# Performance work log

Measured on AMD Instinct MI355X. Metric: run time of the kernel, lower is better.

Reference implementation:

```python
import jax, jax.numpy as jnp
import numpy as np

H = 512          # hidden_size
E = 2 * H        # bidirectional embed dim
NH = 8           # attention heads
HD = E // NH     # head dim = 128
SEQ = 10         # hard-coded seq_len in forward
IN = 512         # input_size
OUT = 256        # output_size


def _gru_dir(gi, Whh, bhh, reverse):
    # gi: [B,S,3H] precomputed input-side gate pre-activations
    if reverse:
        gi = gi[:, ::-1]
    B = gi.shape[0]
    h0 = jnp.zeros((B, H), gi.dtype)

    def step(h, gi_t):
        gh = h @ Whh.T + bhh                      # [B,3H]
        ir, iz, inn = jnp.split(gi_t, 3, axis=-1)
        hr, hz, hn = jnp.split(gh, 3, axis=-1)
        r = jax.nn.sigmoid(ir + hr)
        z = jax.nn.sigmoid(iz + hz)
        n = jnp.tanh(inn + r * hn)
        h_new = (1.0 - z) * n + z * h
        return h_new, h_new

    _, hs = jax.lax.scan(step, h0, jnp.swapaxes(gi, 0, 1))
    hs = jnp.swapaxes(hs, 0, 1)                   # [B,S,H]
    if reverse:
        hs = hs[:, ::-1]
    return hs


def _bi_gru_layer(x_seq, Wih, Whh, bih, bhh):
    # Wih: [2, 3H, in]; dir 0 = forward, dir 1 = backward
    outs = []
    for d, rev in ((0, False), (1, True)):
        gi = jnp.einsum('bsi,gi->bsg', x_seq, Wih[d]) + bih[d]
        outs.append(_gru_dir(gi, Whh[d], bhh[d], rev))
    return jnp.concatenate(outs, axis=-1)         # [B,S,2H]


def _attention(x, in_proj_w, in_proj_b, out_proj_w, out_proj_b):
    B, S, _ = x.shape
    qkv = x @ in_proj_w.T + in_proj_b             # [B,S,3E]
    q, k, v = jnp.split(qkv, 3, axis=-1)
    q = q.reshape(B, S, NH, HD)
    k = k.reshape(B, S, NH, HD)
    v = v.reshape(B, S, NH, HD)
    scores = jnp.einsum('bqhd,bkhd->bhqk', q, k) / jnp.sqrt(jnp.asarray(HD, x.dtype))
    attn = jax.nn.softmax(scores, axis=-1)
    o = jnp.einsum('bhqk,bkhd->bqhd', attn, v).reshape(B, S, E)
    return o @ out_proj_w.T + out_proj_b


def _forward(x, Wp, bp, Wih0, Whh0, bih0, bhh0, Wih1, Whh1, bih1, bhh1,
             in_proj_w, in_proj_b, out_proj_w, out_proj_b, W1, b1, W2, b2):
    x_proj = x @ Wp.T + bp                        # [B,H]
    phases = 2.0 * np.pi * np.arange(SEQ) / SEQ
    cos = jnp.asarray(np.cos(phases), x.dtype)    # [S]
    sin = jnp.asarray(np.sin(phases), x.dtype)
    rolled = jnp.roll(x_proj, shift=1, axis=-1)
    x_seq = (x_proj[:, None, :] * (1.0 + 0.1 * cos[None, :, None])
             + 0.05 * sin[None, :, None] * rolled[:, None, :])  # [B,S,H]
    h1 = _bi_gru_layer(x_seq, Wih0, Whh0, bih0, bhh0)           # [B,S,2H]
    gru_out = _bi_gru_layer(h1, Wih1, Whh1, bih1, bhh1)         # [B,S,2H]
    attn_out = _attention(gru_out, in_proj_w, in_proj_b, out_proj_w, out_proj_b)
    aggregated = jnp.mean(gru_out + attn_out, axis=1)           # [B,2H]
    hid = jnp.tanh(aggregated @ W1.T + b1)                      # [B,128]
    return hid @ W2.T + b2                                      # [B,OUT]


def setup_inputs() -> dict:
    key = jax.random.key(0)
    ks = jax.random.split(key, 24)
    s = 1.0 / np.sqrt(H)
    u = lambda k, shape: jax.random.uniform(k, shape, jnp.float32, -s, s)
    return {
        'x': jax.random.normal(ks[0], (4096, IN), jnp.float32),
        'Wp': u(ks[1], (H, IN)), 'bp': u(ks[2], (H,)),
        'Wih0': u(ks[3], (2, 3 * H, H)), 'Whh0': u(ks[4], (2, 3 * H, H)),
        'bih0': u(ks[5], (2, 3 * H)), 'bhh0': u(ks[6], (2, 3 * H)),
        'Wih1': u(ks[7], (2, 3 * H, 2 * H)), 'Whh1': u(ks[8], (2, 3 * H, H)),
        'bih1': u(ks[9], (2, 3 * H)), 'bhh1': u(ks[10], (2, 3 * H)),
        'in_proj_w': u(ks[11], (3 * E, E)), 'in_proj_b': u(ks[12], (3 * E,)),
        'out_proj_w': u(ks[13], (E, E)), 'out_proj_b': u(ks[14], (E,)),
        'W1': u(ks[15], (128, E)), 'b1': u(ks[16], (128,)),
        'W2': u(ks[17], (OUT, 128)), 'b2': u(ks[18], (OUT,)),
    }


def reference(x, Wp, bp, Wih0, Whh0, bih0, bhh0, Wih1, Whh1, bih1, bhh1,
              in_proj_w, in_proj_b, out_proj_w, out_proj_b, W1, b1, W2, b2):
    return _forward(x, Wp, bp, Wih0, Whh0, bih0, bhh0, Wih1, Whh1, bih1, bhh1,
                    in_proj_w, in_proj_b, out_proj_w, out_proj_b, W1, b1, W2, b2)
```

## Files before the change

kernel.cpp:

```cpp
#include <hip/hip_runtime.h>
#include <math.h>


#define SEQ 10

typedef unsigned short bf16u;
typedef __attribute__((ext_vector_type(8))) short short8v;
typedef __attribute__((ext_vector_type(4))) float f32x4;

#define AS1 __attribute__((address_space(1)))
#define AS3 __attribute__((address_space(3)))

__device__ __forceinline__ float b2f(bf16u u) {
    union { unsigned int i; float f; } v; v.i = ((unsigned int)u) << 16; return v.f;
}
__device__ __forceinline__ bf16u f2b(float f) {
    union { float f; unsigned int i; } v; v.f = f;
    unsigned int r = (v.i + 0x7FFFu + ((v.i >> 16) & 1u)) >> 16;
    return (bf16u)r;
}
__device__ __forceinline__ float fast_sigm(float x) { return 1.0f / (1.0f + __expf(-x)); }
__device__ __forceinline__ float fast_tanh(float x) {
    float e = __expf(-2.0f * x);
    return 2.0f / (1.0f + e) - 1.0f;
}

__global__ void cvt_f2b(const float* __restrict__ src, bf16u* __restrict__ dst, int n4)
{
    int i = blockIdx.x * 256 + threadIdx.x;
    if (i < n4) {
        float4 v = ((const float4*)src)[i];
        ushort4 u; u.x = f2b(v.x); u.y = f2b(v.y); u.z = f2b(v.z); u.w = f2b(v.w);
        ((ushort4*)dst)[i] = u;
    }
}

template <typename TC>
__global__ __launch_bounds__(512) void gemm_mfma256(
    const bf16u* __restrict__ A, long long sAz, int lda,
    const bf16u* __restrict__ W, long long sWz,
    const float* __restrict__ bias, long long sBz,
    TC* __restrict__ C, long long sCz, int ldc,
    int K, int act)
{
    __shared__ bf16u As[2][256 * 64];
    __shared__ bf16u Ws[2][256 * 64];

    const int z = blockIdx.z;
    A += (long long)z * sAz;
    W += (long long)z * sWz;
    C += (long long)z * sCz;
    const float* bz = bias ? (bias + (long long)z * sBz) : nullptr;

    const int gx = gridDim.x;
    const int nwg = gx * gridDim.y;
    const int orig = blockIdx.y * gx + blockIdx.x;
    const int q = nwg >> 3, rres = nwg & 7;
    const int xcd = orig & 7, loc = orig >> 3;
    const int wgid = (xcd < rres ? xcd * (q + 1) : rres * (q + 1) + (xcd - rres) * q) + loc;
    const int bm = (wgid / gx) * 256;
    const int bn = (wgid % gx) * 256;

    const int tid = threadIdx.x;
    const int lane = tid & 63;
    const int w = tid >> 6;
    const int wm = w >> 2;
    const int wn = w & 3;
    const int l15 = lane & 15;
    const int lk8 = (lane >> 4) * 8;
    const int swz = (l15 & 7) << 3;

    f32x4 acc[8][4];
#pragma unroll
    for (int i = 0; i < 8; ++i)
#pragma unroll
        for (int j = 0; j < 4; ++j)
#pragma unroll
            for (int r = 0; r < 4; ++r) acc[i][j][r] = 0.0f;

    const int srow = lane >> 3;
    const int scol = ((lane & 7) ^ srow) * 8;
    const bf16u* Ag[4];
    const bf16u* Wg[4];
    int loff[4];
#pragma unroll
    for (int p = 0; p < 4; ++p) {
        const int r = p * 64 + w * 8 + srow;
        Ag[p] = A + (long long)(bm + r) * lda + scol;
        Wg[p] = W + (long long)(bn + r) * K + scol;
        loff[p] = (p * 8 + w) * 512;
    }

    auto stage = [&](int kt, int b) {
        const long long k1 = (long long)kt << 6;
#pragma unroll
        for (int p = 0; p < 4; ++p) {
            __builtin_amdgcn_global_load_lds((const AS1 void*)(Ag[p] + k1),
                (AS3 void*)(&As[b][loff[p]]), 16, 0, 0);
            __builtin_amdgcn_global_load_lds((const AS1 void*)(Wg[p] + k1),
                (AS3 void*)(&Ws[b][loff[p]]), 16, 0, 0);
        }
    };
    auto compute = [&](int b) {
#pragma unroll
        for (int ks = 0; ks < 2; ++ks) {
            const int ko = (ks * 32 + lk8) ^ swz;
            short8v af[8], bfr[4];
#pragma unroll
            for (int i = 0; i < 8; ++i)
                af[i] = *(const short8v*)(&As[b][(wm * 128 + i * 16 + l15) * 64 + ko]);
#pragma unroll
            for (int i = 0; i < 4; ++i)
                bfr[i] = *(const short8v*)(&Ws[b][(wn * 64 + i * 16 + l15) * 64 + ko]);
#pragma unroll
            for (int mi = 0; mi < 8; ++mi)
#pragma unroll
                for (int ni = 0; ni < 4; ++ni)
                    acc[mi][ni] = __builtin_amdgcn_mfma_f32_16x16x32_bf16(
                        af[mi], bfr[ni], acc[mi][ni], 0, 0, 0);
        }
    };

    const int nt = K >> 6;

    stage(0, 0);
    stage(1, 1);

    for (int t = 0; t < nt - 1; ++t) {
        asm volatile("s_waitcnt vmcnt(8)" ::: "memory");
        __builtin_amdgcn_s_barrier();
        asm volatile("" ::: "memory");
        compute(t & 1);
        asm volatile("" ::: "memory");
        __builtin_amdgcn_s_barrier();
        if (t + 2 < nt) stage(t + 2, t & 1);
    }
    asm volatile("s_waitcnt vmcnt(0)" ::: "memory");
    __builtin_amdgcn_s_barrier();
    compute((nt - 1) & 1);

    const int r0 = (lane >> 4) * 4;
#pragma unroll
    for (int mi = 0; mi < 8; ++mi) {
#pragma unroll
        for (int ni = 0; ni < 4; ++ni) {
            const int col = bn + wn * 64 + ni * 16 + l15;
            float badd = bz ? bz[col] : 0.0f;
#pragma unroll
            for (int r = 0; r < 4; ++r) {
                const long long row = bm + wm * 128 + mi * 16 + r0 + r;
                float v = acc[mi][ni][r] + badd;
                if (act) v = tanhf(v);
                if constexpr (sizeof(TC) == 4) ((float*)C)[row * ldc + col] = v;
                else                           ((bf16u*)C)[row * ldc + col] = f2b(v);
            }
        }
    }
}

template <typename TC>
__global__ __launch_bounds__(256) void gemm_mfma128p(
    const bf16u* __restrict__ A, long long sAz, int lda,
    const bf16u* __restrict__ W, long long sWz,
    const float* __restrict__ bias, long long sBz,
    TC* __restrict__ C, long long sCz, int ldc,
    int K, int act)
{
    __shared__ bf16u As[2][128 * 64];
    __shared__ bf16u Ws[2][128 * 64];

    const int z = blockIdx.z;
    A += (long long)z * sAz;
    W += (long long)z * sWz;
    C += (long long)z * sCz;
    const float* bz = bias ? (bias + (long long)z * sBz) : nullptr;

    const int gx = gridDim.x;
    const int nwg = gx * gridDim.y;
    const int orig = blockIdx.y * gx + blockIdx.x;
    const int q = nwg >> 3, rres = nwg & 7;
    const int xcd = orig & 7, loc = orig >> 3;
    const int wgid = (xcd < rres ? xcd * (q + 1) : rres * (q + 1) + (xcd - rres) * q) + loc;
    const int bm = (wgid / gx) * 128;
    const int bn = (wgid % gx) * 128;

    const int tid = threadIdx.x;
    const int lane = tid & 63;
    const int w = tid >> 6;
    const int wm = w >> 1;
    const int wn = w & 1;
    const int l15 = lane & 15;
    const int lk8 = (lane >> 4) * 8;
    const int swz = (l15 & 7) << 3;

    f32x4 acc[4][4];
#pragma unroll
    for (int i = 0; i < 4; ++i)
#pragma unroll
        for (int j = 0; j < 4; ++j)
#pragma unroll
            for (int r = 0; r < 4; ++r) acc[i][j][r] = 0.0f;

    const int srow = lane >> 3;
    const int scol = ((lane & 7) ^ srow) * 8;
    const bf16u* Ag[4];
    const bf16u* Wg[4];
    int loff[4];
#pragma unroll
    for (int p = 0; p < 4; ++p) {
        const int r = p * 32 + w * 8 + srow;
        Ag[p] = A + (long long)(bm + r) * lda + scol;
        Wg[p] = W + (long long)(bn + r) * K + scol;
        loff[p] = (p * 32 + w * 8) * 64;
    }

    auto stage = [&](int kt, int b) {
        const long long k1 = (long long)kt << 6;
#pragma unroll
        for (int p = 0; p < 4; ++p) {
            __builtin_amdgcn_global_load_lds((const AS1 void*)(Ag[p] + k1),
                (AS3 void*)(&As[b][loff[p]]), 16, 0, 0);
            __builtin_amdgcn_global_load_lds((const AS1 void*)(Wg[p] + k1),
                (AS3 void*)(&Ws[b][loff[p]]), 16, 0, 0);
        }
    };
    auto compute = [&](int b) {
#pragma unroll
        for (int ks = 0; ks < 2; ++ks) {
            const int ko = (ks * 32 + lk8) ^ swz;
            short8v af[4], bfr[4];
#pragma unroll
            for (int i = 0; i < 4; ++i)
                af[i] = *(const short8v*)(&As[b][(wm * 64 + i * 16 + l15) * 64 + ko]);
#pragma unroll
            for (int i = 0; i < 4; ++i)
                bfr[i] = *(const short8v*)(&Ws[b][(wn * 64 + i * 16 + l15) * 64 + ko]);
            __builtin_amdgcn_s_setprio(1);
#pragma unroll
            for (int mi = 0; mi < 4; ++mi)
#pragma unroll
                for (int ni = 0; ni < 4; ++ni)
                    acc[mi][ni] = __builtin_amdgcn_mfma_f32_16x16x32_bf16(
                        af[mi], bfr[ni], acc[mi][ni], 0, 0, 0);
            __builtin_amdgcn_s_setprio(0);
        }
    };

    const int nt = K >> 6;

    stage(0, 0);
    stage(1, 1);

    for (int t = 0; t < nt - 1; ++t) {
        asm volatile("s_waitcnt vmcnt(8)" ::: "memory");
        __builtin_amdgcn_s_barrier();
        asm volatile("" ::: "memory");
        compute(t & 1);
        asm volatile("" ::: "memory");
        __builtin_amdgcn_s_barrier();
        if (t + 2 < nt) stage(t + 2, t & 1);
    }
    asm volatile("s_waitcnt vmcnt(0)" ::: "memory");
    __builtin_amdgcn_s_barrier();
    compute((nt - 1) & 1);

    const int r0 = (lane >> 4) * 4;
#pragma unroll
    for (int mi = 0; mi < 4; ++mi) {
#pragma unroll
        for (int ni = 0; ni < 4; ++ni) {
            const int col = bn + wn * 64 + ni * 16 + l15;
            float badd = bz ? bz[col] : 0.0f;
#pragma unroll
            for (int r = 0; r < 4; ++r) {
                const long long row = bm + wm * 64 + mi * 16 + r0 + r;
                float v = acc[mi][ni][r] + badd;
                if (act) v = tanhf(v);
                if constexpr (sizeof(TC) == 4) ((float*)C)[row * ldc + col] = v;
                else                           ((bf16u*)C)[row * ldc + col] = f2b(v);
            }
        }
    }
}

template <typename TC>
__global__ __launch_bounds__(256) void gemm_mfma(
    const bf16u* __restrict__ A, long long sAz, int lda,
    const bf16u* __restrict__ W, long long sWz,
    const float* __restrict__ bias, long long sBz,
    TC* __restrict__ C, long long sCz, int ldc,
    int K, int act)
{
    __shared__ bf16u As[128 * 64];
    __shared__ bf16u Ws[128 * 64];

    const int z = blockIdx.z;
    A += (long long)z * sAz;
    W += (long long)z * sWz;
    C += (long long)z * sCz;
    const float* bz = bias ? (bias + (long long)z * sBz) : nullptr;

    const int gx = gridDim.x;
    const int nwg = gx * gridDim.y;
    const int orig = blockIdx.y * gx + blockIdx.x;
    const int q = nwg >> 3, rres = nwg & 7;
    const int xcd = orig & 7, loc = orig >> 3;
    const int wgid = (xcd < rres ? xcd * (q + 1) : rres * (q + 1) + (xcd - rres) * q) + loc;
    const int bm = (wgid / gx) * 128;
    const int bn = (wgid % gx) * 128;

    const int tid = threadIdx.x;
    const int lane = tid & 63;
    const int wave = tid >> 6;
    const int wr = (wave >> 1) * 64;
    const int wc = (wave & 1) * 64;
    const int l15 = lane & 15;
    const int lk8 = (lane >> 4) * 8;

    f32x4 acc[4][4];
#pragma unroll
    for (int i = 0; i < 4; ++i)
#pragma unroll
        for (int j = 0; j < 4; ++j)
#pragma unroll
            for (int r = 0; r < 4; ++r) acc[i][j][r] = 0.0f;

    const int sr = wave * 32 + (lane >> 3);
    const int sc = (lane & 7) * 8;
    const bf16u* Ag = A + (long long)(bm + sr) * lda + sc;
    const bf16u* Wg = W + (long long)(bn + sr) * K + sc;
    bf16u* Al = As + wave * 32 * 64;
    bf16u* Wl = Ws + wave * 32 * 64;

    for (int k0 = 0; k0 < K; k0 += 64) {
#pragma unroll
        for (int p = 0; p < 4; ++p) {
            __builtin_amdgcn_global_load_lds(
                (const AS1 void*)(Ag + k0 + (long long)(8 * p) * lda),
                (AS3 void*)(Al + 8 * p * 64), 16, 0, 0);
            __builtin_amdgcn_global_load_lds(
                (const AS1 void*)(Wg + k0 + (long long)(8 * p) * K),
                (AS3 void*)(Wl + 8 * p * 64), 16, 0, 0);
        }
        __syncthreads();
#pragma unroll
        for (int ks = 0; ks < 2; ++ks) {
            short8v af[4], bfr[4];
#pragma unroll
            for (int i = 0; i < 4; ++i)
                af[i] = *(const short8v*)(As + (wr + i * 16 + l15) * 64 + ks * 32 + lk8);
#pragma unroll
            for (int i = 0; i < 4; ++i)
                bfr[i] = *(const short8v*)(Ws + (wc + i * 16 + l15) * 64 + ks * 32 + lk8);
#pragma unroll
            for (int mi = 0; mi < 4; ++mi)
#pragma unroll
                for (int ni = 0; ni < 4; ++ni)
                    acc[mi][ni] = __builtin_amdgcn_mfma_f32_16x16x32_bf16(
                        af[mi], bfr[ni], acc[mi][ni], 0, 0, 0);
        }
        __syncthreads();
    }

    const int r0 = (lane >> 4) * 4;
#pragma unroll
    for (int mi = 0; mi < 4; ++mi) {
#pragma unroll
        for (int ni = 0; ni < 4; ++ni) {
            const int col = bn + wc + ni * 16 + l15;
            float badd = bz ? bz[col] : 0.0f;
#pragma unroll
            for (int r = 0; r < 4; ++r) {
                const long long row = bm + wr + mi * 16 + r0 + r;
                float v = acc[mi][ni][r] + badd;
                if (act) v = tanhf(v);
                if constexpr (sizeof(TC) == 4) ((float*)C)[row * ldc + col] = v;
                else                           ((bf16u*)C)[row * ldc + col] = f2b(v);
            }
        }
    }
}

template <int LAYER, bool FIRST>
__global__ __launch_bounds__(256) void gru_step(
    const bf16u* __restrict__ Hb,
    const bf16u* __restrict__ Whh,
    const float* __restrict__ bhh,
    const bf16u* __restrict__ P0,
    const bf16u* __restrict__ P1,
    const float* __restrict__ bih,
    const bf16u* __restrict__ GIT,
    const float* __restrict__ hprev,
    float* __restrict__ hnext,
    bf16u* __restrict__ hnextb,
    bf16u* __restrict__ hout,
    int t, int CB)
{
    __shared__ bf16u As[2][64 * 64];
    __shared__ bf16u Ws[2][96 * 64];

    const int z = blockIdx.z;
    const int bn = blockIdx.x * 32;
    const int bm = blockIdx.y * 64;
    const int tid = threadIdx.x;
    const int lane = tid & 63;
    const int wave = tid >> 6;
    const int wm = wave >> 1;
    const int wn = wave & 1;
    const int l15 = lane & 15;
    const int lk8 = (lane >> 4) * 8;
    const int swz = (l15 & 7) << 3;

    f32x4 acc[3][2];
#pragma unroll
    for (int g = 0; g < 3; ++g)
#pragma unroll
        for (int i = 0; i < 2; ++i)
#pragma unroll
            for (int r = 0; r < 4; ++r) acc[g][i][r] = 0.0f;

    if constexpr (!FIRST) {
        const bf16u* hsrc = Hb + (long long)z * CB * 512;
        const bf16u* wsrc = Whh + (long long)z * 1536 * 512;

        const int srow = lane >> 3;
        const int sc = ((lane & 7) ^ srow) * 8;
        const bf16u* Ag = hsrc + (long long)(bm + 16 * wave + srow) * 512 + sc;
        const bf16u* Wg[3];
#pragma unroll
        for (int p = 0; p < 3; ++p) {
            const int lr = 24 * wave + 8 * p + srow;
            const int g = lr >> 5, c = lr & 31;
            Wg[p] = wsrc + (long long)(g * 512 + bn + c) * 512 + sc;
        }

        auto stage = [&](int kt, int b) {
            const long long k0 = (long long)kt << 6;
#pragma unroll
            for (int p = 0; p < 2; ++p)
                __builtin_amdgcn_global_load_lds(
                    (const AS1 void*)(Ag + k0 + (long long)(8 * p) * 512),
                    (AS3 void*)(&As[b][(16 * wave + 8 * p) * 64]), 16, 0, 0);
#pragma unroll
            for (int p = 0; p < 3; ++p)
                __builtin_amdgcn_global_load_lds(
                    (const AS1 void*)(Wg[p] + k0),
                    (AS3 void*)(&Ws[b][(24 * wave + 8 * p) * 64]), 16, 0, 0);
        };
        auto compute = [&](int b) {
#pragma unroll
            for (int ks = 0; ks < 2; ++ks) {
                const int ko = (ks * 32 + lk8) ^ swz;
                short8v af[2], bf[3];
#pragma unroll
                for (int mi = 0; mi < 2; ++mi)
                    af[mi] = *(const short8v*)(&As[b][(wm * 32 + mi * 16 + l15) * 64 + ko]);
#pragma unroll
                for (int g = 0; g < 3; ++g)
                    bf[g] = *(const short8v*)(&Ws[b][(g * 32 + wn * 16 + l15) * 64 + ko]);
                __builtin_amdgcn_s_setprio(1);
#pragma unroll
                for (int g = 0; g < 3; ++g)
#pragma unroll
                    for (int mi = 0; mi < 2; ++mi)
                        acc[g][mi] = __builtin_amdgcn_mfma_f32_16x16x32_bf16(
                            af[mi], bf[g], acc[g][mi], 0, 0, 0);
                __builtin_amdgcn_s_setprio(0);
            }
        };

        stage(0, 0);
        stage(1, 1);
        for (int kt = 0; kt < 7; ++kt) {
            asm volatile("s_waitcnt vmcnt(5)" ::: "memory");
            __builtin_amdgcn_s_barrier();
            asm volatile("" ::: "memory");
            compute(kt & 1);
            asm volatile("" ::: "memory");
            __builtin_amdgcn_s_barrier();
            if (kt + 2 < 8) stage(kt + 2, kt & 1);
        }
        asm volatile("s_waitcnt vmcnt(0)" ::: "memory");
        __builtin_amdgcn_s_barrier();
        compute(1);
    }

    const int r0 = (lane >> 4) * 4;
    const int s = z ? (SEQ - 1 - t) : t;
    float c0 = 0.0f, c1 = 0.0f;
    if (LAYER == 0) {
        float ph = 0.6283185307179586f * (float)s;
        c0 = 1.0f + 0.1f * cosf(ph);
        c1 = 0.05f * sinf(ph);
    }

    const int j = bn + wn * 16 + l15;
    const float bh0 = bhh[z * 1536 + j];
    const float bh1 = bhh[z * 1536 + 512 + j];
    const float bh2 = bhh[z * 1536 + 1024 + j];
    float bi0 = 0, bi1 = 0, bi2 = 0;
    if (LAYER == 0) {
        bi0 = bih[z * 1536 + j];
        bi1 = bih[z * 1536 + 512 + j];
        bi2 = bih[z * 1536 + 1024 + j];
    }

#pragma unroll
    for (int mi = 0; mi < 2; ++mi) {
#pragma unroll
        for (int rr = 0; rr < 4; ++rr) {
            const int m = bm + wm * 32 + mi * 16 + r0 + rr;
            float gr = acc[0][mi][rr] + bh0;
            float gz = acc[1][mi][rr] + bh1;
            float gn = acc[2][mi][rr] + bh2;
            float ir, iz, inn;
            if (LAYER == 0) {
                const bf16u* p0 = P0 + (long long)m * 3072 + z * 1536 + j;
                const bf16u* p1 = P1 + (long long)m * 3072 + z * 1536 + j;
                ir  = c0 * b2f(p0[0])    + c1 * b2f(p1[0])    + bi0;
                iz  = c0 * b2f(p0[512])  + c1 * b2f(p1[512])  + bi1;
                inn = c0 * b2f(p0[1024]) + c1 * b2f(p1[1024]) + bi2;
            } else {
                const bf16u* gi = GIT + (((long long)z * CB + m) * SEQ + s) * 1536 + j;
                ir = b2f(gi[0]); iz = b2f(gi[512]); inn = b2f(gi[1024]);
            }
            const long long ho = ((long long)z * CB + m) * 512 + j;
            float r  = fast_sigm(ir + gr);
            float zz = fast_sigm(iz + gz);
            float n  = fast_tanh(inn + r * gn);
            float hnew;
            if constexpr (FIRST) hnew = (1.0f - zz) * n;
            else                 hnew = (1.0f - zz) * n + zz * hprev[ho];
            hnext[ho]  = hnew;
            hnextb[ho] = f2b(hnew);
            hout[((long long)m * SEQ + s) * 1024 + z * 512 + j] = f2b(hnew);
        }
    }
}

__global__ void roll_b(const bf16u* __restrict__ xp, bf16u* __restrict__ rl)
{
    int idx = blockIdx.x * 256 + threadIdx.x;
    int i = idx & 511;
    int b = idx >> 9;
    rl[(size_t)b * 512 + i] = xp[(size_t)b * 512 + ((i + 511) & 511)];
}

__global__ __launch_bounds__(128) void attn_kernel(const bf16u* __restrict__ qkv,
                                                   bf16u* __restrict__ o)
{
    const int bh = blockIdx.x;
    const int h = bh & 7;
    const int bl = bh >> 3;
    const int tid = threadIdx.x;

    __shared__ float Q[SEQ][128], Kx[SEQ][128], V[SEQ][128], Amat[SEQ][SEQ];

    const bf16u* base = qkv + (size_t)bl * SEQ * 3072 + h * 128;
#pragma unroll
    for (int s = 0; s < SEQ; ++s) {
        Q[s][tid]  = b2f(base[s * 3072 + tid]);
        Kx[s][tid] = b2f(base[s * 3072 + 1024 + tid]);
        V[s][tid]  = b2f(base[s * 3072 + 2048 + tid]);
    }
    __syncthreads();

    if (tid < SEQ * SEQ) {
        int q = tid / SEQ, k = tid % SEQ;
        float acc = 0.0f;
#pragma unroll 8
        for (int d0 = 0; d0 < 128; ++d0) acc += Q[q][d0] * Kx[k][d0];
        Amat[q][k] = acc * 0.08838834764831845f;
    }
    __syncthreads();

    if (tid < SEQ) {
        float m = -1e30f;
#pragma unroll
        for (int k = 0; k < SEQ; ++k) m = fmaxf(m, Amat[tid][k]);
        float e[SEQ], ssum = 0.0f;
#pragma unroll
        for (int k = 0; k < SEQ; ++k) { e[k] = expf(Amat[tid][k] - m); ssum += e[k]; }
        float inv = 1.0f / ssum;
#pragma unroll
        for (int k = 0; k < SEQ; ++k) Amat[tid][k] = e[k] * inv;
    }
    __syncthreads();

    bf16u* ob = o + (size_t)bl * SEQ * 1024 + h * 128;
#pragma unroll
    for (int q = 0; q < SEQ; ++q) {
        float acc = 0.0f;
#pragma unroll
        for (int k = 0; k < SEQ; ++k) acc += Amat[q][k] * V[k][tid];
        ob[q * 1024 + tid] = f2b(acc);
    }
}

__global__ void mean_kernel(const bf16u* __restrict__ go, const bf16u* __restrict__ ao,
                            bf16u* __restrict__ agg)
{
    int idx = blockIdx.x * 256 + threadIdx.x;
    int j4 = (idx & 255) * 4;
    int bl = idx >> 8;
    const bf16u* g = go + (size_t)bl * (SEQ * 1024) + j4;
    const bf16u* a = ao + (size_t)bl * (SEQ * 1024) + j4;
    float s0 = 0, s1 = 0, s2 = 0, s3 = 0;
#pragma unroll
    for (int t = 0; t < SEQ; ++t) {
        ushort4 gv = *(const ushort4*)(g + t * 1024);
        ushort4 av = *(const ushort4*)(a + t * 1024);
        s0 += b2f(gv.x) + b2f(av.x);
        s1 += b2f(gv.y) + b2f(av.y);
        s2 += b2f(gv.z) + b2f(av.z);
        s3 += b2f(gv.w) + b2f(av.w);
    }
    ushort4 u; u.x = f2b(0.1f * s0); u.y = f2b(0.1f * s1); u.z = f2b(0.1f * s2); u.w = f2b(0.1f * s3);
    *(ushort4*)(agg + (size_t)bl * 1024 + j4) = u;
}

extern "C" void kernel_launch(void* const* d_in, const int* in_sizes, int n_in,
                              void* d_out, int out_size, void* d_ws, size_t ws_size,
                              hipStream_t stream)
{
    const float* x    = (const float*)d_in[0];
    const float* Wp   = (const float*)d_in[1];
    const float* bp   = (const float*)d_in[2];
    const float* Wih0 = (const float*)d_in[3];
    const float* Whh0 = (const float*)d_in[4];
    const float* bih0 = (const float*)d_in[5];
    const float* bhh0 = (const float*)d_in[6];
    const float* Wih1 = (const float*)d_in[7];
    const float* Whh1 = (const float*)d_in[8];
    const float* bih1 = (const float*)d_in[9];
    const float* bhh1 = (const float*)d_in[10];
    const float* ipw  = (const float*)d_in[11];
    const float* ipb  = (const float*)d_in[12];
    const float* opw  = (const float*)d_in[13];
    const float* opb  = (const float*)d_in[14];
    const float* W1   = (const float*)d_in[15];
    const float* b1   = (const float*)d_in[16];
    const float* W2   = (const float*)d_in[17];
    const float* b2   = (const float*)d_in[18];
    float* out = (float*)d_out;

    const long long WOVER = 9437184LL;
    const long long WALL  = 24969216LL;
    int CB = 0;
    for (int c = 4096; c >= 128; c >>= 1)
        if (WOVER + (long long)c * 114688 <= (long long)ws_size) { CB = c; break; }
    if (CB == 0) return;
    const bool resident = (WALL + (long long)CB * 114688 <= (long long)ws_size);
    const long long WB = resident ? WALL : WOVER;
    const int CBA = CB / 2;

    bf16u* wreg = (bf16u*)d_ws;
    bf16u *Wpb, *Wih0b, *Whh0b, *Wih1b, *Whh1b, *ipwb, *opwb, *W1b, *W2b;
    if (resident) {
        Wpb   = wreg;
        Wih0b = wreg + 262144;
        Whh0b = wreg + 1835008;
        Wih1b = wreg + 3407872;
        Whh1b = wreg + 6553600;
        ipwb  = wreg + 8126464;
        opwb  = wreg + 11272192;
        W1b   = wreg + 12320768;
        W2b   = wreg + 12451840;
    } else {
        Wpb   = wreg;
        Wih0b = wreg + 262144;
        Whh0b = wreg + 1835008;
        Wih1b = wreg;
        Whh1b = wreg + 3145728;
        ipwb  = wreg;
        opwb  = wreg + 3145728;
        W1b   = wreg + 4194304;
        W2b   = wreg + 4325376;
    }

    char* A0 = (char*)d_ws + WB;
    bf16u* H1c = (bf16u*)A0;
    bf16u* GOc = (bf16u*)(A0 + 20480LL * CB);
    char*  U   = A0 + 40960LL * CB;
    bf16u* P0    = (bf16u*)U;
    bf16u* P1    = (bf16u*)(U + 6144LL * CB);
    bf16u* XB    = (bf16u*)(U + 12288LL * CB);
    bf16u* XPb   = (bf16u*)(U + 13312LL * CB);
    bf16u* RLb   = (bf16u*)(U + 14336LL * CB);
    bf16u* GIT   = (bf16u*)U;
    char*  HC    = U + 61440LL * CB;
    bf16u* QKV   = (bf16u*)U;
    bf16u* OC    = (bf16u*)(U + 61440LL * CB);
    bf16u* AOC   = (bf16u*)A0;
    bf16u* AGGb  = (bf16u*)(A0 + 10240LL * CB);
    bf16u* HIDb  = (bf16u*)(A0 + 12288LL * CB);

    const dim3 blk(256);
    const int MB = CB / 128;

    auto cvt = [&](const float* s, bf16u* d, long long nfloats) {
        int n4 = (int)(nfloats / 4);
        cvt_f2b<<<(n4 + 255) / 256, blk, 0, stream>>>(s, d, n4);
    };

    if (resident) {
        cvt(Wp,   Wpb,   512LL * 512);
        cvt(Wih0, Wih0b, 2LL * 1536 * 512);
        cvt(Whh0, Whh0b, 2LL * 1536 * 512);
        cvt(Wih1, Wih1b, 2LL * 1536 * 1024);
        cvt(Whh1, Whh1b, 2LL * 1536 * 512);
        cvt(ipw,  ipwb,  3072LL * 1024);
        cvt(opw,  opwb,  1024LL * 1024);
        cvt(W1,   W1b,   128LL * 1024);
        cvt(W2,   W2b,   256LL * 128);
    }

    for (int c0 = 0; c0 < 4096; c0 += CB) {
        cvt(x + (long long)c0 * 512, XB, (long long)CB * 512);
        if (!resident) {
            cvt(Wp,   Wpb,   512LL * 512);
            cvt(Wih0, Wih0b, 2LL * 1536 * 512);
            cvt(Whh0, Whh0b, 2LL * 1536 * 512);
        }

        gemm_mfma<bf16u><<<dim3(4, MB, 1), blk, 0, stream>>>(
            XB, 0, 512, Wpb, 0, bp, 0, XPb, 0, 512, 512, 0);
        roll_b<<<CB * 2, blk, 0, stream>>>(XPb, RLb);
        gemm_mfma128p<bf16u><<<dim3(24, MB, 2), blk, 0, stream>>>(
            XPb, (long long)CB * 512, 512, Wih0b, 0, nullptr, 0,
            P0, (long long)CB * 3072, 3072, 512, 0);

        for (int t = 0; t < SEQ; ++t) {
            const int rb = t & 1;
            float* hprev  = (float*)(HC + (long long)rb * 6144 * CB);
            bf16u* Hbr    = (bf16u*)(HC + (long long)rb * 6144 * CB + 4096LL * CB);
            float* hnext  = (float*)(HC + (long long)(1 - rb) * 6144 * CB);
            bf16u* hnextb = (bf16u*)(HC + (long long)(1 - rb) * 6144 * CB + 4096LL * CB);
            if (t == 0)
                gru_step<0, true><<<dim3(16, CB / 64, 2), blk, 0, stream>>>(
                    Hbr, Whh0b, bhh0, P0, P1, bih0, nullptr,
                    hprev, hnext, hnextb, H1c, t, CB);
            else
                gru_step<0, false><<<dim3(16, CB / 64, 2), blk, 0, stream>>>(
                    Hbr, Whh0b, bhh0, P0, P1, bih0, nullptr,
                    hprev, hnext, hnextb, H1c, t, CB);
        }

        if (!resident) {
            cvt(Wih1, Wih1b, 2LL * 1536 * 1024);
            cvt(Whh1, Whh1b, 2LL * 1536 * 512);
        }
        gemm_mfma256<bf16u><<<dim3(6, CB * 10 / 256, 2), dim3(512), 0, stream>>>(
            H1c, 0, 1024, Wih1b, 1536LL * 1024, bih1, 1536,
            GIT, (long long)CB * SEQ * 1536, 1536, 1024, 0);

        for (int t = 0; t < SEQ; ++t) {
            const int rb = t & 1;
            float* hprev  = (float*)(HC + (long long)rb * 6144 * CB);
            bf16u* Hbr    = (bf16u*)(HC + (long long)rb * 6144 * CB + 4096LL * CB);
            float* hnext  = (float*)(HC + (long long)(1 - rb) * 6144 * CB);
            bf16u* hnextb = (bf16u*)(HC + (long long)(1 - rb) * 6144 * CB + 4096LL * CB);
            if (t == 0)
                gru_step<1, true><<<dim3(16, CB / 64, 2), blk, 0, stream>>>(
                    Hbr, Whh1b, bhh1, nullptr, nullptr, nullptr, GIT,
                    hprev, hnext, hnextb, GOc, t, CB);
            else
                gru_step<1, false><<<dim3(16, CB / 64, 2), blk, 0, stream>>>(
                    Hbr, Whh1b, bhh1, nullptr, nullptr, nullptr, GIT,
                    hprev, hnext, hnextb, GOc, t, CB);
        }

        if (!resident) {
            cvt(ipw, ipwb, 3072LL * 1024);
            cvt(opw, opwb, 1024LL * 1024);
            cvt(W1,  W1b,  128LL * 1024);
            cvt(W2,  W2b,  256LL * 128);
        }
        gemm_mfma256<bf16u><<<dim3(12, CB * 10 / 256, 1), dim3(512), 0, stream>>>(
            GOc, 0, 1024, ipwb, 0, ipb, 0, QKV, 0, 3072, 1024, 0);
        for (int a0 = 0; a0 < CB; a0 += CBA) {
            attn_kernel<<<CBA * 8, dim3(128), 0, stream>>>(
                QKV + (long long)a0 * 30720, OC);
            gemm_mfma128p<bf16u><<<dim3(8, CBA * 10 / 128, 1), blk, 0, stream>>>(
                OC, 0, 1024, opwb, 0, opb, 0, AOC, 0, 1024, 1024, 0);
            mean_kernel<<<CBA, blk, 0, stream>>>(
                GOc + (long long)a0 * 10240, AOC, AGGb + (long long)a0 * 1024);
        }
        gemm_mfma<bf16u><<<dim3(1, MB, 1), blk, 0, stream>>>(
            AGGb, 0, 1024, W1b, 0, b1, 0, HIDb, 0, 128, 1024, 1);
        gemm_mfma<float><<<dim3(2, MB, 1), blk, 0, stream>>>(
            HIDb, 0, 128, W2b, 0, b2, 0, out + (long long)c0 * 256, 0, 256, 128, 0);
    }
}
```

Measured before the change: 2.123 ms.

## Average attention output over sequence before out-projection to shrink GEMM

Because the output projection is linear, the mean over the sequence is taken inside the attention kernel, and the out-projection GEMM then runs on one row per batch element instead of ten. The attention output buffer, the chunked attention loop and the per-token AO reads in the mean kernel go away, and the projected result is written in fp32 and added to the GRU-output mean. This cuts the out-projection FLOPs and memory traffic by about the sequence length. It relies on gemm_mfma128p being instantiated with a float output and on the fp32 ATT buffer fitting within the reused region.

```diff
diff --git a/kernel.cpp b/kernel.cpp
--- a/kernel.cpp
+++ b/kernel.cpp
@@ -547,7 +547,7 @@
 }
 
 __global__ __launch_bounds__(128) void attn_kernel(const bf16u* __restrict__ qkv,
-                                                   bf16u* __restrict__ o)
+                                                   bf16u* __restrict__ osum)
 {
     const int bh = blockIdx.x;
     const int h = bh & 7;
@@ -587,35 +587,34 @@
     }
     __syncthreads();
 
-    bf16u* ob = o + (size_t)bl * SEQ * 1024 + h * 128;
+    float os = 0.0f;
 #pragma unroll
     for (int q = 0; q < SEQ; ++q) {
         float acc = 0.0f;
 #pragma unroll
         for (int k = 0; k < SEQ; ++k) acc += Amat[q][k] * V[k][tid];
-        ob[q * 1024 + tid] = f2b(acc);
-    }
-}
-
-__global__ void mean_kernel(const bf16u* __restrict__ go, const bf16u* __restrict__ ao,
-                            bf16u* __restrict__ agg)
+        os += acc;
+    }
+    osum[(size_t)bl * 1024 + h * 128 + tid] = f2b(0.1f * os);
+}
+
+__global__ void gmean_kernel(const bf16u* __restrict__ go, const float* __restrict__ att,
+                             bf16u* __restrict__ agg)
 {
     int idx = blockIdx.x * 256 + threadIdx.x;
     int j4 = (idx & 255) * 4;
     int bl = idx >> 8;
     const bf16u* g = go + (size_t)bl * (SEQ * 1024) + j4;
-    const bf16u* a = ao + (size_t)bl * (SEQ * 1024) + j4;
+    float4 a = *(const float4*)(att + (size_t)bl * 1024 + j4);
     float s0 = 0, s1 = 0, s2 = 0, s3 = 0;
 #pragma unroll
     for (int t = 0; t < SEQ; ++t) {
         ushort4 gv = *(const ushort4*)(g + t * 1024);
-        ushort4 av = *(const ushort4*)(a + t * 1024);
-        s0 += b2f(gv.x) + b2f(av.x);
-        s1 += b2f(gv.y) + b2f(av.y);
-        s2 += b2f(gv.z) + b2f(av.z);
-        s3 += b2f(gv.w) + b2f(av.w);
-    }
-    ushort4 u; u.x = f2b(0.1f * s0); u.y = f2b(0.1f * s1); u.z = f2b(0.1f * s2); u.w = f2b(0.1f * s3);
+        s0 += b2f(gv.x); s1 += b2f(gv.y); s2 += b2f(gv.z); s3 += b2f(gv.w);
+    }
+    ushort4 u;
+    u.x = f2b(0.1f * s0 + a.x); u.y = f2b(0.1f * s1 + a.y);
+    u.z = f2b(0.1f * s2 + a.z); u.w = f2b(0.1f * s3 + a.w);
     *(ushort4*)(agg + (size_t)bl * 1024 + j4) = u;
 }
 
@@ -652,7 +651,6 @@
     if (CB == 0) return;
     const bool resident = (WALL + (long long)CB * 114688 <= (long long)ws_size);
     const long long WB = resident ? WALL : WOVER;
-    const int CBA = CB / 2;
 
     bf16u* wreg = (bf16u*)d_ws;
     bf16u *Wpb, *Wih0b, *Whh0b, *Wih1b, *Whh1b, *ipwb, *opwb, *W1b, *W2b;
@@ -690,8 +688,8 @@
     bf16u* GIT   = (bf16u*)U;
     char*  HC    = U + 61440LL * CB;
     bf16u* QKV   = (bf16u*)U;
-    bf16u* OC    = (bf16u*)(U + 61440LL * CB);
-    bf16u* AOC   = (bf16u*)A0;
+    bf16u* OSUMb = (bf16u*)(U + 61440LL * CB);
+    float* ATT   = (float*)A0;
     bf16u* AGGb  = (bf16u*)(A0 + 10240LL * CB);
     bf16u* HIDb  = (bf16u*)(A0 + 12288LL * CB);
 
@@ -778,14 +776,10 @@
         }
         gemm_mfma256<bf16u><<<dim3(12, CB * 10 / 256, 1), dim3(512), 0, stream>>>(
             GOc, 0, 1024, ipwb, 0, ipb, 0, QKV, 0, 3072, 1024, 0);
-        for (int a0 = 0; a0 < CB; a0 += CBA) {
-            attn_kernel<<<CBA * 8, dim3(128), 0, stream>>>(
-                QKV + (long long)a0 * 30720, OC);
-            gemm_mfma128p<bf16u><<<dim3(8, CBA * 10 / 128, 1), blk, 0, stream>>>(
-                OC, 0, 1024, opwb, 0, opb, 0, AOC, 0, 1024, 1024, 0);
-            mean_kernel<<<CBA, blk, 0, stream>>>(
-                GOc + (long long)a0 * 10240, AOC, AGGb + (long long)a0 * 1024);
-        }
+        attn_kernel<<<CB * 8, dim3(128), 0, stream>>>(QKV, OSUMb);
+        gemm_mfma128p<float><<<dim3(8, MB, 1), blk, 0, stream>>>(
+            OSUMb, 0, 1024, opwb, 0, opb, 0, ATT, 0, 1024, 1024, 0);
+        gmean_kernel<<<CB, blk, 0, stream>>>(GOc, ATT, AGGb);
         gemm_mfma<bf16u><<<dim3(1, MB, 1), blk, 0, stream>>>(
             AGGb, 0, 1024, W1b, 0, b1, 0, HIDb, 0, 128, 1024, 1);
         gemm_mfma<float><<<dim3(2, MB, 1), blk, 0, stream>>>(
```

Measured after the change: 2.056 ms (median of 2 runs). 1.03x faster.
